# Performance work log

Measured on AMD Instinct MI355X. Metric: run time of the kernel, lower is better.

## Reference

```python
import jax, jax.numpy as jnp
import numpy as np

N_PIX = 196608  # 12 * 128**2 (HEALPix nside=128)
F = 32          # filters (Fin == Fout for residual)
DM = 2          # depth multiplier


def _cheb_sep_conv(x, idx, wnb, wd, wp, b):
    """Separable Chebyshev graph conv.
    x: [B,N,F] maps; idx: [N,nb] neighbor indices; wnb: [N,nb] Laplacian weights;
    wd: [K,F,DM] depthwise Chebyshev weights; wp: [F*DM,Fout] pointwise; b: [Fout].
    """
    def L(t):  # sparse Laplacian apply via fixed-degree neighbor gather
        return jnp.einsum('bnjf,nj->bnf', t[:, idx, :], wnb)
    K = wd.shape[0]
    Ts = [x, L(x)]
    for _ in range(K - 2):  # Chebyshev recursion T_k = 2 L T_{k-1} - T_{k-2}
        Ts.append(2.0 * L(Ts[-1]) - Ts[-2])
    T = jnp.stack(Ts, 0)                      # [K,B,N,F]
    y = jnp.einsum('kbnf,kfd->bnfd', T, wd)   # depthwise over Chebyshev orders
    Bb, Nn, Ff, Dd = y.shape
    y = y.reshape(Bb, Nn, Ff * Dd)
    return y @ wp + b                         # pointwise mix to Fout


def _layernorm(x, gamma, beta, eps=1e-6):
    mu = jnp.mean(x, axis=-1, keepdims=True)
    var = jnp.mean(jnp.square(x - mu), axis=-1, keepdims=True)
    return (x - mu) * jax.lax.rsqrt(var + eps) * gamma + beta


def setup_inputs() -> dict:
    key = jax.random.key(0)
    ks = jax.random.split(key, 10)
    inp = {
        'maps': jax.random.normal(ks[0], (1, N_PIX, F), jnp.float32),
        'idx1': jax.random.randint(ks[1], (N_PIX, 8), 0, N_PIX, jnp.int32),
        'w1_nb': jax.random.normal(ks[2], (N_PIX, 8), jnp.float32) * 0.1,
        'idx2': jax.random.randint(ks[3], (N_PIX, 20), 0, N_PIX, jnp.int32),
        'w2_nb': jax.random.normal(ks[4], (N_PIX, 20), jnp.float32) * 0.1,
        'wd1': jax.random.normal(ks[5], (6, F, DM), jnp.float32) * 0.1,
        'wp1': jax.random.normal(ks[6], (F * DM, F), jnp.float32) * 0.1,
        'b1': jnp.zeros((F,), jnp.float32),
        'gamma1': jnp.ones((F,), jnp.float32),
        'beta1': jnp.zeros((F,), jnp.float32),
        'wd2': jax.random.normal(ks[7], (10, F, DM), jnp.float32) * 0.1,
        'wp2': jax.random.normal(ks[8], (F * DM, F), jnp.float32) * 0.1,
        'b2': jnp.zeros((F,), jnp.float32),
        'gamma2': jnp.ones((F,), jnp.float32),
        'beta2': jnp.zeros((F,), jnp.float32),
    }
    return inp


def reference(maps, idx1, w1_nb, idx2, w2_nb, wd1, wp1, b1, gamma1, beta1,
              wd2, wp2, b2, gamma2, beta2):
    res = maps
    x = _cheb_sep_conv(maps, idx1, w1_nb, wd1, wp1, b1)   # K=6, nb=8
    x = jax.nn.relu(x)
    x = _layernorm(x, gamma1, beta1)
    x = _cheb_sep_conv(x, idx2, w2_nb, wd2, wp2, b2)      # K=10, nb=20
    x = jax.nn.relu(x)
    x = _layernorm(x, gamma2, beta2)
    return x + res
```

## Files before the change

kernel.cpp:

```cpp
#include <hip/hip_runtime.h>

constexpr int NPIX = 196608;
constexpr int FF   = 32;
constexpr size_t SLOT = (size_t)NPIX * FF;

typedef short bf16x8 __attribute__((ext_vector_type(8)));
typedef float f32x4  __attribute__((ext_vector_type(4)));

__device__ __forceinline__ float b2f(ushort u) {
    union { float f; unsigned int i; } v; v.i = ((unsigned int)u) << 16; return v.f;
}
__device__ __forceinline__ ushort f2b(float f) {
    union { float f; unsigned int i; } v; v.f = f;
    unsigned int r = v.i + 0x7fffu + ((v.i >> 16) & 1u);
    return (ushort)(r >> 16);
}

__global__ __launch_bounds__(256) void f2b_kernel(const float* __restrict__ src,
                                                  ushort* __restrict__ dst) {
    int i = (blockIdx.x * 256 + threadIdx.x) * 4;
    float4 v = *reinterpret_cast<const float4*>(src + i);
    ushort4 o;
    o.x = f2b(v.x); o.y = f2b(v.y); o.z = f2b(v.z); o.w = f2b(v.w);
    *reinterpret_cast<ushort4*>(dst + i) = o;
}

template<int NB>
__global__ __launch_bounds__(256) void cheb_init2(
    const ushort* __restrict__ Tprev,
    const int*    __restrict__ idx,
    const float*  __restrict__ wnb,
    ushort*       __restrict__ Tout)
{
    int t = blockIdx.x * 256 + threadIdx.x;
    int n = t >> 4;
    int h = t & 15;
    const uint*   Tp  = reinterpret_cast<const uint*>(Tprev);
    const int4*   ip  = reinterpret_cast<const int4*>(idx + (size_t)n * NB);
    const float4* wp4 = reinterpret_cast<const float4*>(wnb + (size_t)n * NB);
    float s0 = 0.f, s1 = 0.f;
#pragma unroll
    for (int j4 = 0; j4 < NB / 4; ++j4) {
        int4   i4 = ip[j4];
        float4 w4 = wp4[j4];
        uint u;
        u = Tp[(size_t)i4.x * 16 + h]; s0 += w4.x * b2f((ushort)u); s1 += w4.x * b2f((ushort)(u >> 16));
        u = Tp[(size_t)i4.y * 16 + h]; s0 += w4.y * b2f((ushort)u); s1 += w4.y * b2f((ushort)(u >> 16));
        u = Tp[(size_t)i4.z * 16 + h]; s0 += w4.z * b2f((ushort)u); s1 += w4.z * b2f((ushort)(u >> 16));
        u = Tp[(size_t)i4.w * 16 + h]; s0 += w4.w * b2f((ushort)u); s1 += w4.w * b2f((ushort)(u >> 16));
    }
    reinterpret_cast<uint*>(Tout)[(size_t)n * 16 + h] =
        ((uint)f2b(s1) << 16) | (uint)f2b(s0);
}

template<int NB>
__global__ __launch_bounds__(256) void cheb_step2(
    const ushort* __restrict__ Tprev,
    const ushort* __restrict__ Told,
    ushort*       __restrict__ Tout,
    const int*    __restrict__ idx,
    const float*  __restrict__ wnb)
{
    int t = blockIdx.x * 256 + threadIdx.x;
    int n = t >> 4;
    int h = t & 15;
    const uint*   Tp  = reinterpret_cast<const uint*>(Tprev);
    const int4*   ip  = reinterpret_cast<const int4*>(idx + (size_t)n * NB);
    const float4* wp4 = reinterpret_cast<const float4*>(wnb + (size_t)n * NB);
    float s0 = 0.f, s1 = 0.f;
#pragma unroll
    for (int j4 = 0; j4 < NB / 4; ++j4) {
        int4   i4 = ip[j4];
        float4 w4 = wp4[j4];
        uint u;
        u = Tp[(size_t)i4.x * 16 + h]; s0 += w4.x * b2f((ushort)u); s1 += w4.x * b2f((ushort)(u >> 16));
        u = Tp[(size_t)i4.y * 16 + h]; s0 += w4.y * b2f((ushort)u); s1 += w4.y * b2f((ushort)(u >> 16));
        u = Tp[(size_t)i4.z * 16 + h]; s0 += w4.z * b2f((ushort)u); s1 += w4.z * b2f((ushort)(u >> 16));
        u = Tp[(size_t)i4.w * 16 + h]; s0 += w4.w * b2f((ushort)u); s1 += w4.w * b2f((ushort)(u >> 16));
    }
    size_t base = (size_t)n * 16 + h;
    uint to = reinterpret_cast<const uint*>(Told)[base];
    float t0 = 2.f * s0 - b2f((ushort)to);
    float t1 = 2.f * s1 - b2f((ushort)(to >> 16));
    reinterpret_cast<uint*>(Tout)[base] = ((uint)f2b(t1) << 16) | (uint)f2b(t0);
}

template<int K, bool RESIDUAL, bool OUT_BF16>
__global__ __launch_bounds__(256) void finish_mfma(
    const ushort* __restrict__ chain,
    const float*  __restrict__ wd,
    const float*  __restrict__ wp,
    const float*  __restrict__ bias,
    const float*  __restrict__ gamma,
    const float*  __restrict__ beta,
    const float*  __restrict__ resid,
    void*         __restrict__ outp)
{
    __shared__ __align__(16) ushort sA[4][16][72];
    __shared__ __align__(16) ushort sB[32][72];

    int tid = threadIdx.x;
    int w = tid >> 6;
    int l = tid & 63;

    for (int i = tid; i < 64 * 32; i += 256) {
        int u = i >> 5, g = i & 31;
        sB[g][u] = f2b(wp[i]);
    }

    int nbase = blockIdx.x * 64 + w * 16;

#pragma unroll
    for (int p = 0; p < 8; ++p) {
        int flat = p * 64 + l;
        int nloc = flat >> 5;
        int f    = flat & 31;
        size_t base = (size_t)(nbase + nloc) * FF + f;
        float a0 = 0.f, a1 = 0.f;
#pragma unroll
        for (int k = 0; k < K; ++k) {
            float tv = b2f(chain[(size_t)k * SLOT + base]);
            float2 wk = *reinterpret_cast<const float2*>(wd + (k * FF + f) * 2);
            a0 += tv * wk.x;
            a1 += tv * wk.y;
        }
        uint packed = ((uint)f2b(a1) << 16) | (uint)f2b(a0);
        reinterpret_cast<uint*>(&sA[w][nloc][0])[f] = packed;
    }
    __syncthreads();

    f32x4 acc0 = {0.f, 0.f, 0.f, 0.f};
    f32x4 acc1 = {0.f, 0.f, 0.f, 0.f};
    int r  = l & 15;
    int ko = (l >> 4) * 8;
#pragma unroll
    for (int kt = 0; kt < 2; ++kt) {
        bf16x8 aF = *reinterpret_cast<const bf16x8*>(&sA[w][r][kt * 32 + ko]);
        bf16x8 b0 = *reinterpret_cast<const bf16x8*>(&sB[r][kt * 32 + ko]);
        bf16x8 b1 = *reinterpret_cast<const bf16x8*>(&sB[16 + r][kt * 32 + ko]);
        acc0 = __builtin_amdgcn_mfma_f32_16x16x32_bf16(aF, b0, acc0, 0, 0, 0);
        acc1 = __builtin_amdgcn_mfma_f32_16x16x32_bf16(aF, b1, acc1, 0, 0, 0);
    }

    float bias_lo = bias[r],  bias_hi = bias[16 + r];
    float gam_lo  = gamma[r], gam_hi  = gamma[16 + r];
    float bet_lo  = beta[r],  bet_hi  = beta[16 + r];

#pragma unroll
    for (int v = 0; v < 4; ++v) {
        acc0[v] = fmaxf(acc0[v] + bias_lo, 0.f);
        acc1[v] = fmaxf(acc1[v] + bias_hi, 0.f);
    }
#pragma unroll
    for (int v = 0; v < 4; ++v) {
        float s1 = acc0[v] + acc1[v];
        float s2 = acc0[v] * acc0[v] + acc1[v] * acc1[v];
#pragma unroll
        for (int m = 1; m < 16; m <<= 1) {
            s1 += __shfl_xor(s1, m);
            s2 += __shfl_xor(s2, m);
        }
        float mu  = s1 * (1.f / 32.f);
        float var = s2 * (1.f / 32.f) - mu * mu;
        float rs  = rsqrtf(var + 1e-6f);
        int n = nbase + (l >> 4) * 4 + v;
        size_t o0 = (size_t)n * FF + r;
        size_t o1 = o0 + 16;
        float z0 = (acc0[v] - mu) * rs * gam_lo + bet_lo;
        float z1 = (acc1[v] - mu) * rs * gam_hi + bet_hi;
        if (RESIDUAL) { z0 += resid[o0]; z1 += resid[o1]; }
        if (OUT_BF16) {
            ((ushort*)outp)[o0] = f2b(z0);
            ((ushort*)outp)[o1] = f2b(z1);
        } else {
            ((float*)outp)[o0] = z0;
            ((float*)outp)[o1] = z1;
        }
    }
}

extern "C" void kernel_launch(void* const* d_in, const int* in_sizes, int n_in,
                              void* d_out, int out_size, void* d_ws, size_t ws_size,
                              hipStream_t stream) {
    const float* maps = (const float*)d_in[0];
    const int*   idx1 = (const int*)  d_in[1];
    const float* w1nb = (const float*)d_in[2];
    const int*   idx2 = (const int*)  d_in[3];
    const float* w2nb = (const float*)d_in[4];
    const float* wd1  = (const float*)d_in[5];
    const float* wp1  = (const float*)d_in[6];
    const float* b1   = (const float*)d_in[7];
    const float* g1   = (const float*)d_in[8];
    const float* be1  = (const float*)d_in[9];
    const float* wd2  = (const float*)d_in[10];
    const float* wp2  = (const float*)d_in[11];
    const float* b2   = (const float*)d_in[12];
    const float* g2   = (const float*)d_in[13];
    const float* be2  = (const float*)d_in[14];
    float* out = (float*)d_out;

    ushort* slots = (ushort*)d_ws;
    ushort* B = slots;
    ushort* A = slots + 4 * SLOT;

    const int stepBlocks = NPIX * 16 / 256;
    const int cvtBlocks  = NPIX * FF / (256 * 4);
    const int finBlocks  = NPIX / 64;

    f2b_kernel<<<cvtBlocks, 256, 0, stream>>>(maps, A);
    cheb_init2<8><<<stepBlocks, 256, 0, stream>>>(A, idx1, w1nb, A + SLOT);
    cheb_step2<8><<<stepBlocks, 256, 0, stream>>>(A + SLOT,     A,              A + 2 * SLOT, idx1, w1nb);
    cheb_step2<8><<<stepBlocks, 256, 0, stream>>>(A + 2 * SLOT, A + SLOT,       A + 3 * SLOT, idx1, w1nb);
    cheb_step2<8><<<stepBlocks, 256, 0, stream>>>(A + 3 * SLOT, A + 2 * SLOT,   A + 4 * SLOT, idx1, w1nb);
    cheb_step2<8><<<stepBlocks, 256, 0, stream>>>(A + 4 * SLOT, A + 3 * SLOT,   A + 5 * SLOT, idx1, w1nb);
    finish_mfma<6, false, true><<<finBlocks, 256, 0, stream>>>(A, wd1, wp1, b1, g1, be1, nullptr, B);

    cheb_init2<20><<<stepBlocks, 256, 0, stream>>>(B, idx2, w2nb, B + SLOT);
    for (int k = 2; k <= 9; ++k)
        cheb_step2<20><<<stepBlocks, 256, 0, stream>>>(
            B + (size_t)(k - 1) * SLOT, B + (size_t)(k - 2) * SLOT,
            B + (size_t)k * SLOT, idx2, w2nb);
    finish_mfma<10, true, false><<<finBlocks, 256, 0, stream>>>(B, wd2, wp2, b2, g2, be2, maps, out);
}
```

Before: 733.7 us.

## Widen Chebyshev gathers to 16-byte loads and fold depthwise weights into GEMM

The Chebyshev step kernels now give each thread 8 channels through uint4 gathers (4 threads per pixel instead of 16). This cuts the number of index and weight loads per pixel and issues wider memory transactions. The finish kernel folds the depthwise Chebyshev weights into the pointwise matrix, precomputed per block in shared memory, and runs a K*32-deep MFMA GEMM straight from the chain slots, dropping the scalar depthwise pass. In exchange, every block recomputes the combined weights, and the folded weights are rounded to bf16 in a different order.

```diff
diff --git a/kernel.cpp b/kernel.cpp
--- a/kernel.cpp
+++ b/kernel.cpp
@@ -7,13 +7,19 @@
 typedef short bf16x8 __attribute__((ext_vector_type(8)));
 typedef float f32x4  __attribute__((ext_vector_type(4)));
 
-__device__ __forceinline__ float b2f(ushort u) {
-    union { float f; unsigned int i; } v; v.i = ((unsigned int)u) << 16; return v.f;
+__device__ __forceinline__ float blo(uint u) {
+    union { float f; uint i; } v; v.i = u << 16; return v.f;
+}
+__device__ __forceinline__ float bhi(uint u) {
+    union { float f; uint i; } v; v.i = u & 0xffff0000u; return v.f;
 }
 __device__ __forceinline__ ushort f2b(float f) {
-    union { float f; unsigned int i; } v; v.f = f;
-    unsigned int r = v.i + 0x7fffu + ((v.i >> 16) & 1u);
+    union { float f; uint i; } v; v.f = f;
+    uint r = v.i + 0x7fffu + ((v.i >> 16) & 1u);
     return (ushort)(r >> 16);
+}
+__device__ __forceinline__ uint pack2(float lo, float hi) {
+    return ((uint)f2b(hi) << 16) | (uint)f2b(lo);
 }
 
 __global__ __launch_bounds__(256) void f2b_kernel(const float* __restrict__ src,
@@ -25,36 +31,8 @@
     *reinterpret_cast<ushort4*>(dst + i) = o;
 }
 
-template<int NB>
-__global__ __launch_bounds__(256) void cheb_init2(
-    const ushort* __restrict__ Tprev,
-    const int*    __restrict__ idx,
-    const float*  __restrict__ wnb,
-    ushort*       __restrict__ Tout)
-{
-    int t = blockIdx.x * 256 + threadIdx.x;
-    int n = t >> 4;
-    int h = t & 15;
-    const uint*   Tp  = reinterpret_cast<const uint*>(Tprev);
-    const int4*   ip  = reinterpret_cast<const int4*>(idx + (size_t)n * NB);
-    const float4* wp4 = reinterpret_cast<const float4*>(wnb + (size_t)n * NB);
-    float s0 = 0.f, s1 = 0.f;
-#pragma unroll
-    for (int j4 = 0; j4 < NB / 4; ++j4) {
-        int4   i4 = ip[j4];
-        float4 w4 = wp4[j4];
-        uint u;
-        u = Tp[(size_t)i4.x * 16 + h]; s0 += w4.x * b2f((ushort)u); s1 += w4.x * b2f((ushort)(u >> 16));
-        u = Tp[(size_t)i4.y * 16 + h]; s0 += w4.y * b2f((ushort)u); s1 += w4.y * b2f((ushort)(u >> 16));
-        u = Tp[(size_t)i4.z * 16 + h]; s0 += w4.z * b2f((ushort)u); s1 += w4.z * b2f((ushort)(u >> 16));
-        u = Tp[(size_t)i4.w * 16 + h]; s0 += w4.w * b2f((ushort)u); s1 += w4.w * b2f((ushort)(u >> 16));
-    }
-    reinterpret_cast<uint*>(Tout)[(size_t)n * 16 + h] =
-        ((uint)f2b(s1) << 16) | (uint)f2b(s0);
-}
-
-template<int NB>
-__global__ __launch_bounds__(256) void cheb_step2(
+template<int NB, bool INIT>
+__global__ __launch_bounds__(256, 4) void cheb_step4(
     const ushort* __restrict__ Tprev,
     const ushort* __restrict__ Told,
     ushort*       __restrict__ Tout,
@@ -62,31 +40,70 @@
     const float*  __restrict__ wnb)
 {
     int t = blockIdx.x * 256 + threadIdx.x;
-    int n = t >> 4;
-    int h = t & 15;
-    const uint*   Tp  = reinterpret_cast<const uint*>(Tprev);
-    const int4*   ip  = reinterpret_cast<const int4*>(idx + (size_t)n * NB);
-    const float4* wp4 = reinterpret_cast<const float4*>(wnb + (size_t)n * NB);
-    float s0 = 0.f, s1 = 0.f;
-#pragma unroll
-    for (int j4 = 0; j4 < NB / 4; ++j4) {
-        int4   i4 = ip[j4];
-        float4 w4 = wp4[j4];
-        uint u;
-        u = Tp[(size_t)i4.x * 16 + h]; s0 += w4.x * b2f((ushort)u); s1 += w4.x * b2f((ushort)(u >> 16));
-        u = Tp[(size_t)i4.y * 16 + h]; s0 += w4.y * b2f((ushort)u); s1 += w4.y * b2f((ushort)(u >> 16));
-        u = Tp[(size_t)i4.z * 16 + h]; s0 += w4.z * b2f((ushort)u); s1 += w4.z * b2f((ushort)(u >> 16));
-        u = Tp[(size_t)i4.w * 16 + h]; s0 += w4.w * b2f((ushort)u); s1 += w4.w * b2f((ushort)(u >> 16));
-    }
-    size_t base = (size_t)n * 16 + h;
-    uint to = reinterpret_cast<const uint*>(Told)[base];
-    float t0 = 2.f * s0 - b2f((ushort)to);
-    float t1 = 2.f * s1 - b2f((ushort)(to >> 16));
-    reinterpret_cast<uint*>(Tout)[base] = ((uint)f2b(t1) << 16) | (uint)f2b(t0);
+    int n = t >> 2;
+    int h = t & 3;
+
+    const int4*   ip = reinterpret_cast<const int4*>(idx + (size_t)n * NB);
+    const float4* wv = reinterpret_cast<const float4*>(wnb + (size_t)n * NB);
+    int4   I[NB / 4];
+    float4 W[NB / 4];
+#pragma unroll
+    for (int j = 0; j < NB / 4; ++j) { I[j] = ip[j]; W[j] = wv[j]; }
+
+    const uint4* Tp = reinterpret_cast<const uint4*>(Tprev);
+    float s0 = 0.f, s1 = 0.f, s2 = 0.f, s3 = 0.f;
+    float s4 = 0.f, s5 = 0.f, s6 = 0.f, s7 = 0.f;
+
+#pragma unroll
+    for (int j = 0; j < NB / 4; ++j) {
+        int4 i4 = I[j]; float4 w4 = W[j];
+        {
+            uint4 u = Tp[(size_t)i4.x * 4 + h];
+            s0 += w4.x * blo(u.x); s1 += w4.x * bhi(u.x);
+            s2 += w4.x * blo(u.y); s3 += w4.x * bhi(u.y);
+            s4 += w4.x * blo(u.z); s5 += w4.x * bhi(u.z);
+            s6 += w4.x * blo(u.w); s7 += w4.x * bhi(u.w);
+        }
+        {
+            uint4 u = Tp[(size_t)i4.y * 4 + h];
+            s0 += w4.y * blo(u.x); s1 += w4.y * bhi(u.x);
+            s2 += w4.y * blo(u.y); s3 += w4.y * bhi(u.y);
+            s4 += w4.y * blo(u.z); s5 += w4.y * bhi(u.z);
+            s6 += w4.y * blo(u.w); s7 += w4.y * bhi(u.w);
+        }
+        {
+            uint4 u = Tp[(size_t)i4.z * 4 + h];
+            s0 += w4.z * blo(u.x); s1 += w4.z * bhi(u.x);
+            s2 += w4.z * blo(u.y); s3 += w4.z * bhi(u.y);
+            s4 += w4.z * blo(u.z); s5 += w4.z * bhi(u.z);
+            s6 += w4.z * blo(u.w); s7 += w4.z * bhi(u.w);
+        }
+        {
+            uint4 u = Tp[(size_t)i4.w * 4 + h];
+            s0 += w4.w * blo(u.x); s1 += w4.w * bhi(u.x);
+            s2 += w4.w * blo(u.y); s3 += w4.w * bhi(u.y);
+            s4 += w4.w * blo(u.z); s5 += w4.w * bhi(u.z);
+            s6 += w4.w * blo(u.w); s7 += w4.w * bhi(u.w);
+        }
+    }
+
+    size_t base = (size_t)n * 4 + h;
+    uint4 o;
+    if (INIT) {
+        o.x = pack2(s0, s1); o.y = pack2(s2, s3);
+        o.z = pack2(s4, s5); o.w = pack2(s6, s7);
+    } else {
+        uint4 told = reinterpret_cast<const uint4*>(Told)[base];
+        o.x = pack2(2.f * s0 - blo(told.x), 2.f * s1 - bhi(told.x));
+        o.y = pack2(2.f * s2 - blo(told.y), 2.f * s3 - bhi(told.y));
+        o.z = pack2(2.f * s4 - blo(told.z), 2.f * s5 - bhi(told.z));
+        o.w = pack2(2.f * s6 - blo(told.w), 2.f * s7 - bhi(told.w));
+    }
+    reinterpret_cast<uint4*>(Tout)[base] = o;
 }
 
 template<int K, bool RESIDUAL, bool OUT_BF16>
-__global__ __launch_bounds__(256) void finish_mfma(
+__global__ __launch_bounds__(256, 4) void finish_gemm(
     const ushort* __restrict__ chain,
     const float*  __restrict__ wd,
     const float*  __restrict__ wp,
@@ -96,50 +113,45 @@
     const float*  __restrict__ resid,
     void*         __restrict__ outp)
 {
-    __shared__ __align__(16) ushort sA[4][16][72];
-    __shared__ __align__(16) ushort sB[32][72];
+    constexpr int KW = K * 32;
+    constexpr int WSTRIDE = KW + 8;
+    __shared__ float swp[64 * 33];
+    __shared__ __align__(16) ushort sW[32][WSTRIDE];
 
     int tid = threadIdx.x;
-    int w = tid >> 6;
-    int l = tid & 63;
+    int wv = tid >> 6, l = tid & 63;
+    int r = l & 15, hi = l >> 4;
+    int nbase = blockIdx.x * 64 + wv * 16;
+
+    bf16x8 aF[K];
+#pragma unroll
+    for (int k = 0; k < K; ++k)
+        aF[k] = *reinterpret_cast<const bf16x8*>(
+            chain + (size_t)k * SLOT + (size_t)(nbase + r) * FF + hi * 8);
 
     for (int i = tid; i < 64 * 32; i += 256) {
         int u = i >> 5, g = i & 31;
-        sB[g][u] = f2b(wp[i]);
-    }
-
-    int nbase = blockIdx.x * 64 + w * 16;
-
-#pragma unroll
-    for (int p = 0; p < 8; ++p) {
-        int flat = p * 64 + l;
-        int nloc = flat >> 5;
-        int f    = flat & 31;
-        size_t base = (size_t)(nbase + nloc) * FF + f;
-        float a0 = 0.f, a1 = 0.f;
-#pragma unroll
-        for (int k = 0; k < K; ++k) {
-            float tv = b2f(chain[(size_t)k * SLOT + base]);
-            float2 wk = *reinterpret_cast<const float2*>(wd + (k * FF + f) * 2);
-            a0 += tv * wk.x;
-            a1 += tv * wk.y;
-        }
-        uint packed = ((uint)f2b(a1) << 16) | (uint)f2b(a0);
-        reinterpret_cast<uint*>(&sA[w][nloc][0])[f] = packed;
+        swp[u * 33 + g] = wp[i];
+    }
+    __syncthreads();
+
+    for (int i = tid; i < 32 * KW; i += 256) {
+        int g = i / KW, kf = i - g * KW;
+        int f = kf & 31;
+        float2 wdv = *reinterpret_cast<const float2*>(wd + (size_t)kf * 2);
+        float w2 = wdv.x * swp[(2 * f) * 33 + g] + wdv.y * swp[(2 * f + 1) * 33 + g];
+        sW[g][kf] = f2b(w2);
     }
     __syncthreads();
 
     f32x4 acc0 = {0.f, 0.f, 0.f, 0.f};
     f32x4 acc1 = {0.f, 0.f, 0.f, 0.f};
-    int r  = l & 15;
-    int ko = (l >> 4) * 8;
-#pragma unroll
-    for (int kt = 0; kt < 2; ++kt) {
-        bf16x8 aF = *reinterpret_cast<const bf16x8*>(&sA[w][r][kt * 32 + ko]);
-        bf16x8 b0 = *reinterpret_cast<const bf16x8*>(&sB[r][kt * 32 + ko]);
-        bf16x8 b1 = *reinterpret_cast<const bf16x8*>(&sB[16 + r][kt * 32 + ko]);
-        acc0 = __builtin_amdgcn_mfma_f32_16x16x32_bf16(aF, b0, acc0, 0, 0, 0);
-        acc1 = __builtin_amdgcn_mfma_f32_16x16x32_bf16(aF, b1, acc1, 0, 0, 0);
+#pragma unroll
+    for (int k = 0; k < K; ++k) {
+        bf16x8 b0 = *reinterpret_cast<const bf16x8*>(&sW[r][k * 32 + hi * 8]);
+        bf16x8 b1 = *reinterpret_cast<const bf16x8*>(&sW[16 + r][k * 32 + hi * 8]);
+        acc0 = __builtin_amdgcn_mfma_f32_16x16x32_bf16(aF[k], b0, acc0, 0, 0, 0);
+        acc1 = __builtin_amdgcn_mfma_f32_16x16x32_bf16(aF[k], b1, acc1, 0, 0, 0);
     }
 
     float bias_lo = bias[r],  bias_hi = bias[16 + r];
@@ -163,7 +175,7 @@
         float mu  = s1 * (1.f / 32.f);
         float var = s2 * (1.f / 32.f) - mu * mu;
         float rs  = rsqrtf(var + 1e-6f);
-        int n = nbase + (l >> 4) * 4 + v;
+        int n = nbase + hi * 4 + v;
         size_t o0 = (size_t)n * FF + r;
         size_t o1 = o0 + 16;
         float z0 = (acc0[v] - mu) * rs * gam_lo + bet_lo;
@@ -203,22 +215,22 @@
     ushort* B = slots;
     ushort* A = slots + 4 * SLOT;
 
-    const int stepBlocks = NPIX * 16 / 256;
+    const int stepBlocks = NPIX * 4 / 256;
     const int cvtBlocks  = NPIX * FF / (256 * 4);
     const int finBlocks  = NPIX / 64;
 
     f2b_kernel<<<cvtBlocks, 256, 0, stream>>>(maps, A);
-    cheb_init2<8><<<stepBlocks, 256, 0, stream>>>(A, idx1, w1nb, A + SLOT);
-    cheb_step2<8><<<stepBlocks, 256, 0, stream>>>(A + SLOT,     A,              A + 2 * SLOT, idx1, w1nb);
-    cheb_step2<8><<<stepBlocks, 256, 0, stream>>>(A + 2 * SLOT, A + SLOT,       A + 3 * SLOT, idx1, w1nb);
-    cheb_step2<8><<<stepBlocks, 256, 0, stream>>>(A + 3 * SLOT, A + 2 * SLOT,   A + 4 * SLOT, idx1, w1nb);
-    cheb_step2<8><<<stepBlocks, 256, 0, stream>>>(A + 4 * SLOT, A + 3 * SLOT,   A + 5 * SLOT, idx1, w1nb);
-    finish_mfma<6, false, true><<<finBlocks, 256, 0, stream>>>(A, wd1, wp1, b1, g1, be1, nullptr, B);
-
-    cheb_init2<20><<<stepBlocks, 256, 0, stream>>>(B, idx2, w2nb, B + SLOT);
+    cheb_step4<8, true><<<stepBlocks, 256, 0, stream>>>(A, nullptr, A + SLOT, idx1, w1nb);
+    cheb_step4<8, false><<<stepBlocks, 256, 0, stream>>>(A + SLOT,     A,              A + 2 * SLOT, idx1, w1nb);
+    cheb_step4<8, false><<<stepBlocks, 256, 0, stream>>>(A + 2 * SLOT, A + SLOT,       A + 3 * SLOT, idx1, w1nb);
+    cheb_step4<8, false><<<stepBlocks, 256, 0, stream>>>(A + 3 * SLOT, A + 2 * SLOT,   A + 4 * SLOT, idx1, w1nb);
+    cheb_step4<8, false><<<stepBlocks, 256, 0, stream>>>(A + 4 * SLOT, A + 3 * SLOT,   A + 5 * SLOT, idx1, w1nb);
+    finish_gemm<6, false, true><<<finBlocks, 256, 0, stream>>>(A, wd1, wp1, b1, g1, be1, nullptr, B);
+
+    cheb_step4<20, true><<<stepBlocks, 256, 0, stream>>>(B, nullptr, B + SLOT, idx2, w2nb);
     for (int k = 2; k <= 9; ++k)
-        cheb_step2<20><<<stepBlocks, 256, 0, stream>>>(
+        cheb_step4<20, false><<<stepBlocks, 256, 0, stream>>>(
             B + (size_t)(k - 1) * SLOT, B + (size_t)(k - 2) * SLOT,
             B + (size_t)k * SLOT, idx2, w2nb);
-    finish_mfma<10, true, false><<<finBlocks, 256, 0, stream>>>(B, wd2, wp2, b2, g2, be2, maps, out);
-}
+    finish_gemm<10, true, false><<<finBlocks, 256, 0, stream>>>(B, wd2, wp2, b2, g2, be2, maps, out);
+}
```

After: 766.2 us. 1.04x slower.
